# Kernel optimization log

Measured on AMD Instinct MI355X. Metric: run time of the kernel, lower is better.

The kernel has to match this reference:

```python
import jax, jax.numpy as jnp
import numpy as np

BATCH = 4096
IN_FEATURES = 8192
OUT_FEATURES = 8192
N_GROUPS = 1024  # non-overlapping value ranges partitioning [-4, 4]


def setup_inputs() -> dict:
    key = jax.random.key(0)
    k1, k2, k3 = jax.random.split(key, 3)
    x = jax.random.normal(k1, (BATCH, IN_FEATURES), dtype=jnp.float32)
    # Range index metadata (sorted by min, non-overlapping, as _build_range_index assumes)
    edges = jnp.linspace(-4.0, 4.0, N_GROUPS + 1).astype(jnp.float32)
    mins = edges[:-1]
    maxs = edges[1:]
    # Each group owns a full IN_FEATURES-wide weight row in the flat NVMe buffer
    start_pos = jnp.zeros((N_GROUPS,), dtype=jnp.int32)
    sizes = jnp.full((N_GROUPS,), IN_FEATURES, dtype=jnp.int32)
    offsets = (jnp.arange(N_GROUPS, dtype=jnp.int32) * IN_FEATURES)
    weights_flat = jax.random.normal(k2, (N_GROUPS * IN_FEATURES,), dtype=jnp.float32) * 0.02
    # Which output neurons have any metadata entry (others are skipped -> stay 0)
    out_mask = jax.random.randint(k3, (OUT_FEATURES,), 0, 2) > 0
    return {"x": x, "weights_flat": weights_flat, "mins": mins, "maxs": maxs,
            "start_pos": start_pos, "offsets": offsets, "sizes": sizes, "out_mask": out_mask}


def reference(x, weights_flat, mins, maxs, start_pos, offsets, sizes, out_mask):
    B, IN = x.shape
    OUT = out_mask.shape[0]
    G = mins.shape[0]
    # input_val per position: x[:, i].mean() (equals x[0, i] when B == 1)
    val = jnp.mean(x, axis=0)  # [IN]
    # binary search over sorted non-overlapping [min, max] ranges
    g = jnp.searchsorted(mins, val, side='right').astype(jnp.int32) - 1  # [IN]
    gc = jnp.clip(g, 0, G - 1)
    hit = (g >= 0) & (val >= mins[gc]) & (val <= maxs[gc])
    # weight lookup: pos_in_group = in_idx - start_pos, bounds-checked
    pos = jnp.arange(IN, dtype=jnp.int32) - start_pos[gc]
    pos_ok = (pos >= 0) & (pos < sizes[gc])
    idx = jnp.clip(offsets[gc] + pos, 0, weights_flat.shape[0] - 1)
    w = jnp.where(hit & pos_ok, weights_flat[idx], jnp.float32(0))
    # inner MAC loop is independent of out_idx -> same scalar for every covered neuron
    s = jnp.sum(val * w)
    row0 = jnp.where(out_mask, s, jnp.float32(0))  # [OUT]
    out = jnp.zeros((B, OUT), dtype=x.dtype).at[0].set(row0)
    return out
```

## Files before the change

kernel.cpp:

```cpp
#include <hip/hip_runtime.h>

#define BATCH 4096
#define IN_F 8192
#define OUT_F 8192
#define NG 1024
#define NW (NG * IN_F)
#define ROWS_PER_BLK 16

__global__ __launch_bounds__(256) void colsum_kernel(const float* __restrict__ x,
                                                     float* __restrict__ colsum) {
    const int col4 = (blockIdx.x * 256 + threadIdx.x);
    const int row0 = blockIdx.y * ROWS_PER_BLK;
    const float4* __restrict__ xp = (const float4*)x;
    const int stride4 = IN_F / 4;
    long long base = (long long)row0 * stride4 + col4;
    float4 v[ROWS_PER_BLK];
#pragma unroll
    for (int r = 0; r < ROWS_PER_BLK; ++r)
        v[r] = xp[base + (long long)r * stride4];
    float a0 = 0.f, a1 = 0.f, a2 = 0.f, a3 = 0.f;
#pragma unroll
    for (int r = 0; r < ROWS_PER_BLK; ++r) {
        a0 += v[r].x; a1 += v[r].y; a2 += v[r].z; a3 += v[r].w;
    }
    float* dst = colsum + col4 * 4;
    atomicAdd(dst + 0, a0);
    atomicAdd(dst + 1, a1);
    atomicAdd(dst + 2, a2);
    atomicAdd(dst + 3, a3);
}

__global__ __launch_bounds__(256) void scalar_kernel(const float* __restrict__ colsum,
                                                     const float* __restrict__ mins,
                                                     const float* __restrict__ maxs,
                                                     const int* __restrict__ start_pos,
                                                     const int* __restrict__ offsets,
                                                     const int* __restrict__ sizes,
                                                     const float* __restrict__ wflat,
                                                     const unsigned char* __restrict__ mask_raw,
                                                     float* __restrict__ ws_scalars) {
    __shared__ float smins[NG];
    __shared__ float sred[256];
    __shared__ int sflag[256];
    const int t = threadIdx.x;
    for (int i = t; i < NG; i += 256) smins[i] = mins[i];

    const int* mi = (const int*)mask_raw;
    int ok = 1;
#pragma unroll
    for (int i = 0; i < 8; ++i) {
        int v = mi[t * 8 + i];
        ok &= (v == 0 || v == 1) ? 1 : 0;
    }
    sflag[t] = ok;
    __syncthreads();

    float local = 0.f;
    for (int j = t; j < IN_F; j += 256) {
        float val = colsum[j] * (1.0f / (float)BATCH);
        int lo = 0, hi = NG;
        while (lo < hi) {
            int mid = (lo + hi) >> 1;
            if (smins[mid] <= val) lo = mid + 1; else hi = mid;
        }
        int g = lo - 1;
        if (g >= 0) {
            if (val >= smins[g] && val <= maxs[g]) {
                int pos = j - start_pos[g];
                if (pos >= 0 && pos < sizes[g]) {
                    long long idx = (long long)offsets[g] + (long long)pos;
                    if (idx < 0) idx = 0;
                    if (idx > (long long)(NW - 1)) idx = NW - 1;
                    local += val * wflat[idx];
                }
            }
        }
    }
    sred[t] = local;
    __syncthreads();
    for (int ofs = 128; ofs > 0; ofs >>= 1) {
        if (t < ofs) { sred[t] += sred[t + ofs]; sflag[t] &= sflag[t + ofs]; }
        __syncthreads();
    }
    if (t == 0) {
        ws_scalars[0] = sred[0];
        ((int*)ws_scalars)[1] = sflag[0];
    }
}

__global__ __launch_bounds__(256) void row0_kernel(const unsigned char* __restrict__ mask_raw,
                                                   const float* __restrict__ ws_scalars,
                                                   float* __restrict__ out) {
    const int j = blockIdx.x * 256 + threadIdx.x;
    if (j >= OUT_F) return;
    const float s = ws_scalars[0];
    const int mask_is_i32 = ((const int*)ws_scalars)[1];
    int m = mask_is_i32 ? ((const int*)mask_raw)[j] : (int)mask_raw[j];
    out[j] = m ? s : 0.0f;
}

extern "C" void kernel_launch(void* const* d_in, const int* in_sizes, int n_in,
                              void* d_out, int out_size, void* d_ws, size_t ws_size,
                              hipStream_t stream) {
    const float* x          = (const float*)d_in[0];
    const float* wflat      = (const float*)d_in[1];
    const float* mins       = (const float*)d_in[2];
    const float* maxs       = (const float*)d_in[3];
    const int*   start_pos  = (const int*)d_in[4];
    const int*   offsets    = (const int*)d_in[5];
    const int*   sizes      = (const int*)d_in[6];
    const unsigned char* mask = (const unsigned char*)d_in[7];
    float* out = (float*)d_out;

    float* colsum     = (float*)d_ws;
    float* ws_scalars = colsum + IN_F;

    hipMemsetAsync(colsum, 0, IN_F * sizeof(float), stream);
    hipMemsetAsync(d_out, 0, (size_t)out_size * sizeof(float), stream);

    colsum_kernel<<<dim3(IN_F / (256 * 4), BATCH / ROWS_PER_BLK), 256, 0, stream>>>(x, colsum);
    scalar_kernel<<<1, 256, 0, stream>>>(colsum, mins, maxs, start_pos, offsets, sizes,
                                         wflat, mask, ws_scalars);
    row0_kernel<<<OUT_F / 256, 256, 0, stream>>>(mask, ws_scalars, out);
}
```

Measured before the change: 328.3 us.

## Parallelize scalar lookup across blocks and fuse output zeroing into row writer

The single-block scalar kernel becomes 32 blocks, each handling 256 input columns with group metadata staged in shared memory, and partial sums combined by an atomicAdd. The separate hipMemset of the 128 MB output is removed; a grid-stride float4 kernel now writes zeros everywhere and the masked scalar into row 0. This targets the serial latency of the one-block reduction and the extra memset launch, at the cost of a nondeterministic float summation order. Block 0 still computes the mask-dtype flag, but nothing orders it before the other blocks finish, which only matters for the next kernel, and that runs after the whole kernel completes.

```diff
diff --git a/kernel.cpp b/kernel.cpp
--- a/kernel.cpp
+++ b/kernel.cpp
@@ -40,63 +40,91 @@
                                                      const unsigned char* __restrict__ mask_raw,
                                                      float* __restrict__ ws_scalars) {
     __shared__ float smins[NG];
+    __shared__ int sstart[NG];
+    __shared__ int soffs[NG];
+    __shared__ int ssize[NG];
     __shared__ float sred[256];
-    __shared__ int sflag[256];
     const int t = threadIdx.x;
-    for (int i = t; i < NG; i += 256) smins[i] = mins[i];
-
-    const int* mi = (const int*)mask_raw;
-    int ok = 1;
-#pragma unroll
-    for (int i = 0; i < 8; ++i) {
-        int v = mi[t * 8 + i];
-        ok &= (v == 0 || v == 1) ? 1 : 0;
+    for (int i = t; i < NG; i += 256) {
+        smins[i]  = mins[i];
+        sstart[i] = start_pos[i];
+        soffs[i]  = offsets[i];
+        ssize[i]  = sizes[i];
     }
-    sflag[t] = ok;
     __syncthreads();
 
+    const int j = blockIdx.x * 256 + t;
+    float val = colsum[j] * (1.0f / (float)BATCH);
+    int lo = 0, hi = NG;
+    while (lo < hi) {
+        int mid = (lo + hi) >> 1;
+        if (smins[mid] <= val) lo = mid + 1; else hi = mid;
+    }
+    int g = lo - 1;
     float local = 0.f;
-    for (int j = t; j < IN_F; j += 256) {
-        float val = colsum[j] * (1.0f / (float)BATCH);
-        int lo = 0, hi = NG;
-        while (lo < hi) {
-            int mid = (lo + hi) >> 1;
-            if (smins[mid] <= val) lo = mid + 1; else hi = mid;
-        }
-        int g = lo - 1;
-        if (g >= 0) {
-            if (val >= smins[g] && val <= maxs[g]) {
-                int pos = j - start_pos[g];
-                if (pos >= 0 && pos < sizes[g]) {
-                    long long idx = (long long)offsets[g] + (long long)pos;
-                    if (idx < 0) idx = 0;
-                    if (idx > (long long)(NW - 1)) idx = NW - 1;
-                    local += val * wflat[idx];
-                }
-            }
+    if (g >= 0 && val >= smins[g] && val <= maxs[g]) {
+        int pos = j - sstart[g];
+        if (pos >= 0 && pos < ssize[g]) {
+            long long idx = (long long)soffs[g] + (long long)pos;
+            if (idx < 0) idx = 0;
+            if (idx > (long long)(NW - 1)) idx = NW - 1;
+            local = val * wflat[idx];
         }
     }
     sred[t] = local;
     __syncthreads();
     for (int ofs = 128; ofs > 0; ofs >>= 1) {
-        if (t < ofs) { sred[t] += sred[t + ofs]; sflag[t] &= sflag[t + ofs]; }
+        if (t < ofs) sred[t] += sred[t + ofs];
         __syncthreads();
     }
-    if (t == 0) {
-        ws_scalars[0] = sred[0];
-        ((int*)ws_scalars)[1] = sflag[0];
+    if (t == 0) atomicAdd(&ws_scalars[0], sred[0]);
+
+    if (blockIdx.x == 0) {
+        const int* mi = (const int*)mask_raw;
+        int ok = 1;
+#pragma unroll
+        for (int i = 0; i < 8; ++i) {
+            int v = mi[t * 8 + i];
+            ok &= (v == 0 || v == 1) ? 1 : 0;
+        }
+        __syncthreads();
+        ((unsigned long long)0);
+        __shared__ int sflag[256];
+        sflag[t] = ok;
+        __syncthreads();
+        for (int ofs = 128; ofs > 0; ofs >>= 1) {
+            if (t < ofs) sflag[t] &= sflag[t + ofs];
+            __syncthreads();
+        }
+        if (t == 0) ((int*)ws_scalars)[1] = sflag[0];
     }
 }
 
-__global__ __launch_bounds__(256) void row0_kernel(const unsigned char* __restrict__ mask_raw,
-                                                   const float* __restrict__ ws_scalars,
-                                                   float* __restrict__ out) {
-    const int j = blockIdx.x * 256 + threadIdx.x;
-    if (j >= OUT_F) return;
+__global__ __launch_bounds__(256) void out_kernel(const unsigned char* __restrict__ mask_raw,
+                                                  const float* __restrict__ ws_scalars,
+                                                  float4* __restrict__ out4) {
+    const long long total4 = (long long)BATCH * OUT_F / 4;
+    const long long stride = (long long)gridDim.x * blockDim.x;
+    long long i = (long long)blockIdx.x * blockDim.x + threadIdx.x;
     const float s = ws_scalars[0];
     const int mask_is_i32 = ((const int*)ws_scalars)[1];
-    int m = mask_is_i32 ? ((const int*)mask_raw)[j] : (int)mask_raw[j];
-    out[j] = m ? s : 0.0f;
+    for (; i < total4; i += stride) {
+        float4 v = make_float4(0.f, 0.f, 0.f, 0.f);
+        if (i < OUT_F / 4) {
+            const int j = (int)i * 4;
+            int m0, m1, m2, m3;
+            if (mask_is_i32) {
+                const int* mi = (const int*)mask_raw;
+                m0 = mi[j]; m1 = mi[j + 1]; m2 = mi[j + 2]; m3 = mi[j + 3];
+            } else {
+                m0 = mask_raw[j]; m1 = mask_raw[j + 1];
+                m2 = mask_raw[j + 2]; m3 = mask_raw[j + 3];
+            }
+            v.x = m0 ? s : 0.f; v.y = m1 ? s : 0.f;
+            v.z = m2 ? s : 0.f; v.w = m3 ? s : 0.f;
+        }
+        out4[i] = v;
+    }
 }
 
 extern "C" void kernel_launch(void* const* d_in, const int* in_sizes, int n_in,
@@ -110,16 +138,14 @@
     const int*   offsets    = (const int*)d_in[5];
     const int*   sizes      = (const int*)d_in[6];
     const unsigned char* mask = (const unsigned char*)d_in[7];
-    float* out = (float*)d_out;
 
     float* colsum     = (float*)d_ws;
     float* ws_scalars = colsum + IN_F;
 
-    hipMemsetAsync(colsum, 0, IN_F * sizeof(float), stream);
-    hipMemsetAsync(d_out, 0, (size_t)out_size * sizeof(float), stream);
+    hipMemsetAsync(colsum, 0, IN_F * sizeof(float) + 8, stream);
 
     colsum_kernel<<<dim3(IN_F / (256 * 4), BATCH / ROWS_PER_BLK), 256, 0, stream>>>(x, colsum);
-    scalar_kernel<<<1, 256, 0, stream>>>(colsum, mins, maxs, start_pos, offsets, sizes,
-                                         wflat, mask, ws_scalars);
-    row0_kernel<<<OUT_F / 256, 256, 0, stream>>>(mask, ws_scalars, out);
+    scalar_kernel<<<IN_F / 256, 256, 0, stream>>>(colsum, mins, maxs, start_pos, offsets,
+                                                  sizes, wflat, mask, ws_scalars);
+    out_kernel<<<2048, 256, 0, stream>>>(mask, ws_scalars, (float4*)d_out);
 }
```

Result: faster. 275.5 us (-16.1%).
